# Optimization experiments

Hardware: AMD Instinct MI355X
Metric: run time of the kernel (lower is better)

The kernel has to match this reference:

```python
import jax, jax.numpy as jnp
import numpy as np

RATIO = 2
KSIZE = 12
PAD = KSIZE // 2 - RATIO // 2  # 5


def setup_inputs() -> dict:
    key = jax.random.key(0)
    k1, k2 = jax.random.split(key)
    x = jax.random.normal(k1, (4, 64, 256, 256), dtype=jnp.float32)
    # fixed anti-aliasing filter buffer (kaiser-jinc in original); random stand-in
    filt = jax.random.normal(k2, (KSIZE, KSIZE), dtype=jnp.float32)
    return {"x": x, "filt": filt}


def reference(x, filt):
    B, C, H, W = x.shape
    # reflect pad
    xp = jnp.pad(x, ((0, 0), (0, 0), (PAD, PAD), (PAD, PAD)), mode="reflect")
    # depthwise conv_transpose2d(stride=RATIO, groups=C) == conv with
    # lhs_dilation=RATIO, full padding (k-1), spatially flipped kernel
    w = jnp.broadcast_to(filt[::-1, ::-1][None, None], (C, 1, KSIZE, KSIZE))
    y = jax.lax.conv_general_dilated(
        xp, w,
        window_strides=(1, 1),
        padding=[(KSIZE - 1, KSIZE - 1)] * 2,
        lhs_dilation=(RATIO, RATIO),
        dimension_numbers=("NCHW", "OIHW", "NCHW"),
        feature_group_count=C,
    )
    y = (RATIO ** 2) * y
    pl = PAD * RATIO + (KSIZE - RATIO) // 2       # 15
    pr = PAD * RATIO + (KSIZE - RATIO + 1) // 2   # 15
    return y[..., pl:-pr, pl:-pr]
```

## Files before the change

kernel.cpp:

```cpp
#include <hip/hip_runtime.h>


#define S 40
#define TW 1552

typedef float v2f __attribute__((ext_vector_type(2)));
typedef float v4f __attribute__((ext_vector_type(4)));
typedef __attribute__((address_space(3))) void lds_t;
typedef __attribute__((address_space(1))) const void gm_t;

__global__ void filter_prep(const float* __restrict__ filt, float* __restrict__ ws)
{
    int t = threadIdx.x;
    if (t < 144) {
        int n = t % 6, m = (t / 6) % 6, px = (t / 36) & 1, py = t / 72;
        float f = 4.0f * filt[(11 - py - 2 * m) * 12 + (11 - px - 2 * n)];
        ws[2 * t]     = f;
        ws[2 * t + 1] = f;
    }
}

__global__ __launch_bounds__(256, 4) void upsample2d_kernel(
    const float* __restrict__ x, const v2f* __restrict__ ftp,
    float* __restrict__ out)
{
    __shared__ float s_in[2 * TW];

    const int tx = threadIdx.x, ty = threadIdx.y;
    const int w    = ty >> 2;
    const int lane = (ty & 3) * 16 + tx;
    const int bc0 = blockIdx.z;
    const int boy = blockIdx.y, box = blockIdx.x;

    int goff[6];
    #pragma unroll
    for (int k = 0; k < 6; ++k) {
        int j = w * 384 + 64 * k + lane;
        if (j > 1519) j = 1519;
        int r = (j * 1639) >> 16;
        int c = j - r * 40;
        int gy = boy * 32 - 3 + r, gx = box * 32 - 3 + c;
        gy = gy < 0 ? -gy : gy;  gy = gy > 255 ? 510 - gy : gy;
        gx = gx < 0 ? -gx : gx;  gx = gx > 255 ? 510 - gx : gx;
        goff[k] = gy * 256 + gx;
    }

    const float* x0 = x + (size_t)bc0 * 65536;
    const float* x1 = x0 + (size_t)128 * 65536;

    #pragma unroll
    for (int k = 0; k < 6; ++k)
        __builtin_amdgcn_global_load_lds((gm_t*)(x0 + goff[k]),
                                         (lds_t*)(s_in + w * 384 + 64 * k), 4, 0, 0);
    #pragma unroll
    for (int k = 0; k < 6; ++k)
        __builtin_amdgcn_global_load_lds((gm_t*)(x1 + goff[k]),
                                         (lds_t*)(s_in + TW + w * 384 + 64 * k), 4, 0, 0);

    const int xb  = (2 * ty) * S + 2 * tx;
    const int OY0 = boy * 64 + 4 * ty;
    const int OX  = box * 64 + 4 * tx;

    auto tile = [&](const int sbase, float* oc) {
        v2f accp[4][2] = {};
        #pragma unroll
        for (int r = 0; r < 8; ++r) {
            const int rb = sbase + xb + r * S;
            v2f e[4], o[3];
            #pragma unroll
            for (int j = 0; j < 4; ++j)
                e[j] = *reinterpret_cast<const v2f*>(&s_in[rb + 2 * j]);
            #pragma unroll
            for (int j = 0; j < 3; ++j) {
                o[j].x = s_in[rb + 2 * j + 1];
                o[j].y = s_in[rb + 2 * j + 2];
            }
            #pragma unroll
            for (int qy = 0; qy < 2; ++qy)
            #pragma unroll
            for (int py = 0; py < 2; ++py) {
                const int m = r - qy - py;
                if (m >= 0 && m <= 5) {
                    #pragma unroll
                    for (int px = 0; px < 2; ++px)
                    #pragma unroll
                    for (int n = 0; n < 6; ++n) {
                        const int c = px + n;
                        const v2f xp = (c & 1) ? o[(c - 1) >> 1] : e[c >> 1];
                        const v2f f2 = ftp[((py * 2 + px) * 6 + m) * 6 + n];
                        accp[2 * qy + py][px] =
                            __builtin_elementwise_fma(xp, f2, accp[2 * qy + py][px]);
                    }
                }
            }
        }
        #pragma unroll
        for (int oy = 0; oy < 4; ++oy) {
            v4f v = (v4f){accp[oy][0].x, accp[oy][1].x,
                          accp[oy][0].y, accp[oy][1].y};
            __builtin_nontemporal_store(v,
                reinterpret_cast<v4f*>(&oc[(size_t)(OY0 + oy) * 512 + OX]));
        }
    };

    asm volatile("s_waitcnt vmcnt(6)" ::: "memory");
    __builtin_amdgcn_sched_barrier(0);
    __builtin_amdgcn_s_barrier();
    __builtin_amdgcn_sched_barrier(0);
    tile(0, out + (size_t)bc0 * 262144);

    asm volatile("s_waitcnt vmcnt(16)" ::: "memory");
    __builtin_amdgcn_sched_barrier(0);
    __builtin_amdgcn_s_barrier();
    __builtin_amdgcn_sched_barrier(0);
    tile(TW, out + (size_t)(bc0 + 128) * 262144);
}

extern "C" void kernel_launch(void* const* d_in, const int* in_sizes, int n_in,
                              void* d_out, int out_size, void* d_ws, size_t ws_size,
                              hipStream_t stream) {
    const float* x    = (const float*)d_in[0];
    const float* filt = (const float*)d_in[1];
    float* out = (float*)d_out;
    float* ws  = (float*)d_ws;

    filter_prep<<<dim3(1), dim3(256), 0, stream>>>(filt, ws);

    dim3 grid(8, 8, 128);
    dim3 block(16, 16, 1);
    upsample2d_kernel<<<grid, block, 0, stream>>>(x, (const v2f*)ws, out);
}
```

Baseline: 79.81 us.

## Process four batch planes per block with double-buffered LDS staging

Each block now handles one channel across all four batches rather than two planes. Async global-to-LDS loads for the next plane are issued into the freed buffer while the other buffer is being computed, and the grid is halved. The aim is to overlap load latency with compute and amortise index setup across more work. The cost is fewer blocks (4096), which lowers parallelism and latency hiding across blocks, and the hand-counted vmcnt values must match the load and store counts exactly.

```diff
diff --git a/kernel.cpp b/kernel.cpp
--- a/kernel.cpp
+++ b/kernel.cpp
@@ -20,6 +20,17 @@
     }
 }
 
+#define WAIT_BAR(N)                                          \
+    asm volatile("s_waitcnt vmcnt(" #N ")" ::: "memory");    \
+    __builtin_amdgcn_sched_barrier(0);                       \
+    __builtin_amdgcn_s_barrier();                            \
+    __builtin_amdgcn_sched_barrier(0);
+
+#define BAR_ONLY()                                           \
+    __builtin_amdgcn_sched_barrier(0);                       \
+    __builtin_amdgcn_s_barrier();                            \
+    __builtin_amdgcn_sched_barrier(0);
+
 __global__ __launch_bounds__(256, 4) void upsample2d_kernel(
     const float* __restrict__ x, const v2f* __restrict__ ftp,
     float* __restrict__ out)
@@ -29,7 +40,7 @@
     const int tx = threadIdx.x, ty = threadIdx.y;
     const int w    = ty >> 2;
     const int lane = (ty & 3) * 16 + tx;
-    const int bc0 = blockIdx.z;
+    const int ch  = blockIdx.z;
     const int boy = blockIdx.y, box = blockIdx.x;
 
     int goff[6];
@@ -45,23 +56,22 @@
         goff[k] = gy * 256 + gx;
     }
 
-    const float* x0 = x + (size_t)bc0 * 65536;
-    const float* x1 = x0 + (size_t)128 * 65536;
+    const float* xc = x + (size_t)ch * 65536;
 
-    #pragma unroll
-    for (int k = 0; k < 6; ++k)
-        __builtin_amdgcn_global_load_lds((gm_t*)(x0 + goff[k]),
-                                         (lds_t*)(s_in + w * 384 + 64 * k), 4, 0, 0);
-    #pragma unroll
-    for (int k = 0; k < 6; ++k)
-        __builtin_amdgcn_global_load_lds((gm_t*)(x1 + goff[k]),
-                                         (lds_t*)(s_in + TW + w * 384 + 64 * k), 4, 0, 0);
+    auto stage = [&](int b, float* buf) {
+        const float* src = xc + (size_t)b * 4194304;
+        #pragma unroll
+        for (int k = 0; k < 6; ++k)
+            __builtin_amdgcn_global_load_lds((gm_t*)(src + goff[k]),
+                                             (lds_t*)(buf + w * 384 + 64 * k), 4, 0, 0);
+    };
 
     const int xb  = (2 * ty) * S + 2 * tx;
     const int OY0 = boy * 64 + 4 * ty;
     const int OX  = box * 64 + 4 * tx;
 
-    auto tile = [&](const int sbase, float* oc) {
+    auto tile = [&](const int sbase, int b) {
+        float* oc = out + (size_t)(b * 64 + ch) * 262144;
         v2f accp[4][2] = {};
         #pragma unroll
         for (int r = 0; r < 8; ++r) {
@@ -103,17 +113,26 @@
         }
     };
 
-    asm volatile("s_waitcnt vmcnt(6)" ::: "memory");
-    __builtin_amdgcn_sched_barrier(0);
-    __builtin_amdgcn_s_barrier();
-    __builtin_amdgcn_sched_barrier(0);
-    tile(0, out + (size_t)bc0 * 262144);
+    stage(0, s_in);
+    stage(1, s_in + TW);
 
-    asm volatile("s_waitcnt vmcnt(16)" ::: "memory");
-    __builtin_amdgcn_sched_barrier(0);
-    __builtin_amdgcn_s_barrier();
-    __builtin_amdgcn_sched_barrier(0);
-    tile(TW, out + (size_t)(bc0 + 128) * 262144);
+    WAIT_BAR(6)
+    tile(0, 0);
+
+    BAR_ONLY()
+    stage(2, s_in);
+
+    WAIT_BAR(22)
+    tile(TW, 1);
+
+    BAR_ONLY()
+    stage(3, s_in + TW);
+
+    WAIT_BAR(22)
+    tile(0, 2);
+
+    WAIT_BAR(16)
+    tile(TW, 3);
 }
 
 extern "C" void kernel_launch(void* const* d_in, const int* in_sizes, int n_in,
@@ -126,7 +145,7 @@
 
     filter_prep<<<dim3(1), dim3(256), 0, stream>>>(filt, ws);
 
-    dim3 grid(8, 8, 128);
+    dim3 grid(8, 8, 64);
     dim3 block(16, 16, 1);
     upsample2d_kernel<<<grid, block, 0, stream>>>(x, (const v2f*)ws, out);
 }
```

Result: slower. 84.86 us (+6.3%).
